# Kernel tuning notes

Measured on AMD Instinct MI355X. Metric: run time of the kernel, lower is better.

The kernel has to match this reference:

```python
import jax, jax.numpy as jnp
import numpy as np

NUM_EXPERTS = 8
TOP_K = 2
D = 2048   # hidden_dim
F = 4096   # ffn_dim


def setup_inputs() -> dict:
    key = jax.random.key(0)
    k0, k1, k2, k3, k4 = jax.random.split(key, 5)
    hidden_states = jax.random.normal(k0, (2, 2048, D), dtype=jnp.float32)
    gate_w = jax.random.normal(k1, (NUM_EXPERTS, D), dtype=jnp.float32) * 0.02
    w1 = jax.random.normal(k2, (NUM_EXPERTS, F, D), dtype=jnp.float32) * 0.02
    w2 = jax.random.normal(k3, (NUM_EXPERTS, D, F), dtype=jnp.float32) * 0.02
    w3 = jax.random.normal(k4, (NUM_EXPERTS, F, D), dtype=jnp.float32) * 0.02
    return {"hidden_states": hidden_states, "gate_w": gate_w, "w1": w1, "w2": w2, "w3": w3}


def reference(hidden_states, gate_w, w1, w2, w3):
    B, S, Dm = hidden_states.shape
    h = hidden_states.reshape(-1, Dm)                      # [T, D]
    router_logits = h @ gate_w.T                           # [T, E]
    rw = jax.nn.softmax(router_logits.astype(jnp.float32), axis=-1)
    rw, selected = jax.lax.top_k(rw, TOP_K)                # [T, K], [T, K]
    rw = rw / jnp.sum(rw, axis=-1, keepdims=True)
    rw = rw.astype(h.dtype)
    final = jnp.zeros_like(h)
    for e in range(NUM_EXPERTS):                            # small fixed loop over experts
        w = jnp.sum(rw * (selected == e), axis=1, keepdims=True)  # [T, 1]
        gated = jax.nn.silu(h @ w1[e].T) * (h @ w3[e].T)   # [T, F]
        final = final + (gated @ w2[e].T) * w              # [T, D]
    return final.reshape(B, S, Dm), router_logits
```

## Files before the change

kernel.cpp:

```cpp
#include <hip/hip_runtime.h>
#include <hip/hip_bf16.h>
#include <stdint.h>

#define NE 8
#define TKK 2
#define DD 2048
#define FF 4096
#define TT 4096
#define CONV13 2048
#define CONV2  1024

typedef __attribute__((ext_vector_type(8))) short bf16x8;
typedef __attribute__((ext_vector_type(4))) float f32x4;

__device__ inline unsigned short f2bf(float f) {
  union { float f; unsigned u; } x; x.f = f;
  unsigned r = x.u + 0x7fffu + ((x.u >> 16) & 1u);
  return (unsigned short)(r >> 16);
}

__device__ inline bf16x8 cvt8(float4 a, float4 b) {
  union { unsigned short h[8]; bf16x8 v; } x;
  x.h[0] = f2bf(a.x); x.h[1] = f2bf(a.y); x.h[2] = f2bf(a.z); x.h[3] = f2bf(a.w);
  x.h[4] = f2bf(b.x); x.h[5] = f2bf(b.y); x.h[6] = f2bf(b.z); x.h[7] = f2bf(b.w);
  return x.v;
}

__device__ __forceinline__ void conv8(const float* __restrict__ src,
                                      unsigned short* __restrict__ dst, long i) {
  float4 a = *(const float4*)(src + i);
  float4 b = *(const float4*)(src + i + 4);
  union { unsigned short h[8]; uint4 v; } o;
  o.h[0] = f2bf(a.x); o.h[1] = f2bf(a.y); o.h[2] = f2bf(a.z); o.h[3] = f2bf(a.w);
  o.h[4] = f2bf(b.x); o.h[5] = f2bf(b.y); o.h[6] = f2bf(b.z); o.h[7] = f2bf(b.w);
  *(uint4*)(dst + i) = o.v;
}

#define GLL16(g, l) __builtin_amdgcn_global_load_lds( \
    (__attribute__((address_space(1))) void*)(void*)(g), \
    (__attribute__((address_space(3))) void*)(l), 16, 0, 0)

__device__ __forceinline__ void router_one(
    int t, int lane, const float* __restrict__ h, const float* __restrict__ gw,
    float* __restrict__ logits, unsigned short* __restrict__ hb,
    int* __restrict__ counts, int* __restrict__ tok_idx,
    int* __restrict__ sel_e, int* __restrict__ sel_slot, float* __restrict__ sel_w) {
  const float4* hr = (const float4*)(h + (size_t)t * DD);
  float4 hv[8];
  float acc[NE];
#pragma unroll
  for (int e = 0; e < NE; e++) acc[e] = 0.f;
#pragma unroll
  for (int j = 0; j < 8; j++) hv[j] = hr[j * 64 + lane];
  ushort4* hbr = (ushort4*)(hb + (size_t)t * DD);
#pragma unroll
  for (int j = 0; j < 8; j++) {
    ushort4 o;
    o.x = f2bf(hv[j].x); o.y = f2bf(hv[j].y); o.z = f2bf(hv[j].z); o.w = f2bf(hv[j].w);
    hbr[j * 64 + lane] = o;
  }
#pragma unroll
  for (int e = 0; e < NE; e++) {
    const float4* g = (const float4*)(gw + (size_t)e * DD);
    float a = 0.f;
#pragma unroll
    for (int j = 0; j < 8; j++) {
      float4 gv = g[j * 64 + lane];
      a += hv[j].x * gv.x + hv[j].y * gv.y + hv[j].z * gv.z + hv[j].w * gv.w;
    }
    acc[e] = a;
  }
#pragma unroll
  for (int e = 0; e < NE; e++) {
    float v = acc[e];
#pragma unroll
    for (int o = 32; o > 0; o >>= 1) v += __shfl_xor(v, o, 64);
    acc[e] = v;
  }
  if (lane == 0) {
#pragma unroll
    for (int e = 0; e < NE; e++) logits[(size_t)t * NE + e] = acc[e];
    int e1 = 0; float m1 = acc[0];
#pragma unroll
    for (int e = 1; e < NE; e++) if (acc[e] > m1) { m1 = acc[e]; e1 = e; }
    int e2 = -1; float m2 = -3.4e38f;
#pragma unroll
    for (int e = 0; e < NE; e++) if (e != e1 && acc[e] > m2) { m2 = acc[e]; e2 = e; }
    float s = expf(m2 - m1);
    float wa = 1.f / (1.f + s);
    float wb = s * wa;
    int s1 = atomicAdd(&counts[e1], 1);
    tok_idx[e1 * TT + s1] = t;
    int s2 = atomicAdd(&counts[e2], 1);
    tok_idx[e2 * TT + s2] = t;
    sel_e[2 * t] = e1; sel_slot[2 * t] = s1; sel_w[2 * t] = wa;
    sel_e[2 * t + 1] = e2; sel_slot[2 * t + 1] = s2; sel_w[2 * t + 1] = wb;
  }
}

__global__ void router_kernel(const float* __restrict__ h, const float* __restrict__ gw,
                              float* __restrict__ logits, unsigned short* __restrict__ hb,
                              int* __restrict__ counts, int* __restrict__ tok_idx,
                              int* __restrict__ sel_e, int* __restrict__ sel_slot,
                              float* __restrict__ sel_w) {
  router_one(blockIdx.x, threadIdx.x, h, gw, logits, hb, counts, tok_idx, sel_e, sel_slot, sel_w);
}

__global__ __launch_bounds__(256) void prep_kernel(
    const float* __restrict__ h, const float* __restrict__ gw,
    float* __restrict__ logits, unsigned short* __restrict__ hb,
    int* __restrict__ counts, int* __restrict__ tok_idx,
    int* __restrict__ sel_e, int* __restrict__ sel_slot, float* __restrict__ sel_w,
    const float* __restrict__ w1, unsigned short* __restrict__ w1b,
    const float* __restrict__ w3, unsigned short* __restrict__ w3b) {
  if (blockIdx.x < CONV13) {
    long nw = (long)NE * FF * DD;
    long i = ((long)blockIdx.x * 256 + threadIdx.x) * 8;
    long stride = (long)CONV13 * 256 * 8;
    for (; i < 2 * nw; i += stride) {
      if (i < nw) conv8(w1, w1b, i);
      else        conv8(w3, w3b, i - nw);
    }
    return;
  }
  int b = blockIdx.x - CONV13;
  router_one(b * 4 + (threadIdx.x >> 6), threadIdx.x & 63,
             h, gw, logits, hb, counts, tok_idx, sel_e, sel_slot, sel_w);
}

__global__ void offsets_kernel(const int* __restrict__ counts, int* __restrict__ offsets) {
  if (threadIdx.x == 0) {
    int r = 0;
    for (int e = 0; e < NE; e++) { offsets[e] = r; r += counts[e]; }
  }
}

__global__ __launch_bounds__(256) void gemm1c_kernel(
    const unsigned short* __restrict__ w1b, const unsigned short* __restrict__ w3b,
    const unsigned short* __restrict__ hb, const int* __restrict__ tok_idx,
    const int* __restrict__ counts, const int* __restrict__ offsets,
    unsigned short* __restrict__ gated,
    const float* __restrict__ w2f, unsigned short* __restrict__ w2b) {
  __shared__ __align__(16) char lds[32768];
  char* Ab = lds;
  char* B1 = lds + 16384;
  char* B3 = lds + 24576;

  if (blockIdx.x < CONV2) {
    long nw = (long)NE * FF * DD;
    long i = ((long)blockIdx.x * 256 + threadIdx.x) * 8;
    long stride = (long)CONV2 * 256 * 8;
    for (; i < nw; i += stride) conv8(w2f, w2b, i);
    return;
  }

  int bid = blockIdx.x - CONV2;
  int x = bid & 7;
  int rest = bid >> 3;
  int m = rest & 31;
  int q = rest >> 5;
  int p = x + 8 * q;
  int n = p & 63;
  int e = p >> 6;
  int cnt = counts[e];
  int row0 = m * 128;
  if (row0 >= cnt) return;
  int offe = offsets[e];
  int tid = threadIdx.x;

  long asrc[4];
#pragma unroll
  for (int i = 0; i < 4; i++) {
    int r = i * 32 + (tid >> 3);
    int rr = row0 + r; if (rr >= cnt) rr = cnt - 1;
    int tok = tok_idx[e * TT + rr];
    asrc[i] = (long)tok * DD + (((tid & 7) ^ (r & 7)) * 8);
  }
  int fbase = n * 64;
  long ebase = (long)e * FF * DD;
  long bsrc[2];
#pragma unroll
  for (int i = 0; i < 2; i++) {
    int r = i * 32 + (tid >> 3);
    bsrc[i] = ebase + (long)(fbase + r) * DD + (((tid & 7) ^ (r & 7)) * 8);
  }

  f32x4 acc1[4][2], acc3[4][2];
#pragma unroll
  for (int i = 0; i < 4; i++)
#pragma unroll
    for (int j = 0; j < 2; j++) { acc1[i][j] = (f32x4){0,0,0,0}; acc3[i][j] = (f32x4){0,0,0,0}; }

  int wv = tid >> 6;
  int lane = tid & 63;
  int wr = (wv >> 1) * 64;
  int wc = (wv & 1) * 32;
  int lrow = lane & 15;
  int lk4 = lane >> 4;

  for (int k0 = 0; k0 < DD; k0 += 64) {
    if (k0) __syncthreads();
#pragma unroll
    for (int i = 0; i < 4; i++)
      GLL16(hb + asrc[i] + k0, Ab + i * 4096 + tid * 16);
#pragma unroll
    for (int i = 0; i < 2; i++) {
      GLL16(w1b + bsrc[i] + k0, B1 + i * 4096 + tid * 16);
      GLL16(w3b + bsrc[i] + k0, B3 + i * 4096 + tid * 16);
    }
    __syncthreads();
#pragma unroll
    for (int kk = 0; kk < 2; kk++) {
      int kseg = kk * 4 + lk4;
      bf16x8 af[4], b1f[2], b3f[2];
#pragma unroll
      for (int i = 0; i < 4; i++) {
        int row = wr + i * 16 + lrow;
        af[i] = *(const bf16x8*)(Ab + row * 128 + ((kseg ^ (row & 7)) * 16));
      }
#pragma unroll
      for (int j = 0; j < 2; j++) {
        int row = wc + j * 16 + lrow;
        int off = row * 128 + ((kseg ^ (row & 7)) * 16);
        b1f[j] = *(const bf16x8*)(B1 + off);
        b3f[j] = *(const bf16x8*)(B3 + off);
      }
#pragma unroll
      for (int i = 0; i < 4; i++)
#pragma unroll
        for (int j = 0; j < 2; j++) {
          acc1[i][j] = __builtin_amdgcn_mfma_f32_16x16x32_bf16(af[i], b1f[j], acc1[i][j], 0, 0, 0);
          acc3[i][j] = __builtin_amdgcn_mfma_f32_16x16x32_bf16(af[i], b3f[j], acc3[i][j], 0, 0, 0);
        }
    }
  }
  int crow0 = wr + (lane >> 4) * 4;
  int ccol0 = wc + (lane & 15);
#pragma unroll
  for (int i = 0; i < 4; i++)
#pragma unroll
    for (int j = 0; j < 2; j++)
#pragma unroll
      for (int r = 0; r < 4; r++) {
        int trow = crow0 + i * 16 + r;
        if (row0 + trow < cnt) {
          float g = acc1[i][j][r];
          float sg = g / (1.f + __expf(-g));
          float val = sg * acc3[i][j][r];
          gated[(size_t)(offe + row0 + trow) * FF + (fbase + ccol0 + j * 16)] = f2bf(val);
        }
      }
}

__global__ __launch_bounds__(256) void gemm1_kernel_fb(
    const float* __restrict__ w1f, const float* __restrict__ w3f,
    const unsigned short* __restrict__ hb, const int* __restrict__ tok_idx,
    const int* __restrict__ counts, const int* __restrict__ offsets,
    unsigned short* __restrict__ gated) {
  __shared__ __align__(16) char lds[49152];
  char* Ab = lds;
  char* B1 = lds + 16384;
  char* B3 = lds + 32768;

  int bid = blockIdx.x;
  int x = bid & 7;
  int rest = bid >> 3;
  int m = rest & 31;
  int q = rest >> 5;
  int p = x + 8 * q;
  int n = p & 63;
  int e = p >> 6;
  int cnt = counts[e];
  int row0 = m * 128;
  if (row0 >= cnt) return;
  int offe = offsets[e];
  int tid = threadIdx.x;

  long asrc[4];
#pragma unroll
  for (int i = 0; i < 4; i++) {
    int r = i * 32 + (tid >> 3);
    int rr = row0 + r; if (rr >= cnt) rr = cnt - 1;
    int tok = tok_idx[e * TT + rr];
    asrc[i] = (long)tok * DD + (((tid & 7) ^ (r & 7)) * 8);
  }
  int fbase = n * 64;
  long ebase = (long)e * FF * DD;
  long bsrc[4];
#pragma unroll
  for (int i = 0; i < 4; i++) {
    int r = i * 16 + (tid >> 4);
    bsrc[i] = ebase + (long)(fbase + r) * DD + (((tid & 15) ^ (r & 15)) * 4);
  }

  f32x4 acc1[4][2], acc3[4][2];
#pragma unroll
  for (int i = 0; i < 4; i++)
#pragma unroll
    for (int j = 0; j < 2; j++) { acc1[i][j] = (f32x4){0,0,0,0}; acc3[i][j] = (f32x4){0,0,0,0}; }

  int wv = tid >> 6;
  int lane = tid & 63;
  int wr = (wv >> 1) * 64;
  int wc = (wv & 1) * 32;
  int lrow = lane & 15;
  int lk4 = lane >> 4;

  for (int k0 = 0; k0 < DD; k0 += 64) {
    if (k0) __syncthreads();
#pragma unroll
    for (int i = 0; i < 4; i++)
      GLL16(hb + asrc[i] + k0, Ab + i * 4096 + tid * 16);
#pragma unroll
    for (int i = 0; i < 4; i++) {
      GLL16(w1f + bsrc[i] + k0, B1 + i * 4096 + tid * 16);
      GLL16(w3f + bsrc[i] + k0, B3 + i * 4096 + tid * 16);
    }
    __syncthreads();
#pragma unroll
    for (int kk = 0; kk < 2; kk++) {
      int kseg = kk * 4 + lk4;
      int fs = kk * 8 + lk4 * 2;
      bf16x8 af[4], b1f[2], b3f[2];
#pragma unroll
      for (int i = 0; i < 4; i++) {
        int row = wr + i * 16 + lrow;
        af[i] = *(const bf16x8*)(Ab + row * 128 + ((kseg ^ (row & 7)) * 16));
      }
#pragma unroll
      for (int j = 0; j < 2; j++) {
        int row = wc + j * 16 + lrow;
        int rx = row & 15;
        float4 a0 = *(const float4*)(B1 + row * 256 + ((fs ^ rx) * 16));
        float4 a1 = *(const float4*)(B1 + row * 256 + (((fs + 1) ^ rx) * 16));
        b1f[j] = cvt8(a0, a1);
        float4 c0 = *(const float4*)(B3 + row * 256 + ((fs ^ rx) * 16));
        float4 c1 = *(const float4*)(B3 + row * 256 + (((fs + 1) ^ rx) * 16));
        b3f[j] = cvt8(c0, c1);
      }
#pragma unroll
      for (int i = 0; i < 4; i++)
#pragma unroll
        for (int j = 0; j < 2; j++) {
          acc1[i][j] = __builtin_amdgcn_mfma_f32_16x16x32_bf16(af[i], b1f[j], acc1[i][j], 0, 0, 0);
          acc3[i][j] = __builtin_amdgcn_mfma_f32_16x16x32_bf16(af[i], b3f[j], acc3[i][j], 0, 0, 0);
        }
    }
  }
  int crow0 = wr + (lane >> 4) * 4;
  int ccol0 = wc + (lane & 15);
#pragma unroll
  for (int i = 0; i < 4; i++)
#pragma unroll
    for (int j = 0; j < 2; j++)
#pragma unroll
      for (int r = 0; r < 4; r++) {
        int trow = crow0 + i * 16 + r;
        if (row0 + trow < cnt) {
          float g = acc1[i][j][r];
          float sg = g / (1.f + __expf(-g));
          float val = sg * acc3[i][j][r];
          gated[(size_t)(offe + row0 + trow) * FF + (fbase + ccol0 + j * 16)] = f2bf(val);
        }
      }
}

template <bool WB16>
__global__ __launch_bounds__(256) void gemm2_kernel(
    const float* __restrict__ w2f, const unsigned short* __restrict__ w2b,
    const unsigned short* __restrict__ gated,
    const int* __restrict__ counts, const int* __restrict__ offsets,
    float* __restrict__ eout) {
  __shared__ __align__(16) char lds[WB16 ? 32768 : 49152];
  char* Ab = lds;
  char* Bb = lds + 16384;

  int bid = blockIdx.x;
  int x = bid & 7;
  int rest = bid >> 3;
  int m = rest & 31;
  int q = rest >> 5;
  int p = x + 8 * q;
  int n = p & 15;
  int e = p >> 4;
  int cnt = counts[e];
  int row0 = m * 128;
  if (row0 >= cnt) return;
  int offe = offsets[e];
  int tid = threadIdx.x;

  long asrc[4];
#pragma unroll
  for (int i = 0; i < 4; i++) {
    int r = i * 32 + (tid >> 3);
    int rr = row0 + r; if (rr >= cnt) rr = cnt - 1;
    asrc[i] = (long)(offe + rr) * FF + (((tid & 7) ^ (r & 7)) * 8);
  }
  int dbase = n * 128;
  long ebase = (long)e * DD * FF;
  long bsrc[8];
  if constexpr (WB16) {
#pragma unroll
    for (int i = 0; i < 4; i++) {
      int r = i * 32 + (tid >> 3);
      bsrc[i] = ebase + (long)(dbase + r) * FF + (((tid & 7) ^ (r & 7)) * 8);
    }
  } else {
#pragma unroll
    for (int i = 0; i < 8; i++) {
      int r = i * 16 + (tid >> 4);
      bsrc[i] = ebase + (long)(dbase + r) * FF + (((tid & 15) ^ (r & 15)) * 4);
    }
  }

  f32x4 acc[4][4];
#pragma unroll
  for (int i = 0; i < 4; i++)
#pragma unroll
    for (int j = 0; j < 4; j++) acc[i][j] = (f32x4){0,0,0,0};

  int wv = tid >> 6;
  int lane = tid & 63;
  int wr = (wv >> 1) * 64;
  int wc = (wv & 1) * 64;
  int lrow = lane & 15;
  int lk4 = lane >> 4;

  for (int k0 = 0; k0 < FF; k0 += 64) {
    if (k0) __syncthreads();
#pragma unroll
    for (int i = 0; i < 4; i++)
      GLL16(gated + asrc[i] + k0, Ab + i * 4096 + tid * 16);
    if constexpr (WB16) {
#pragma unroll
      for (int i = 0; i < 4; i++)
        GLL16(w2b + bsrc[i] + k0, Bb + i * 4096 + tid * 16);
    } else {
#pragma unroll
      for (int i = 0; i < 8; i++)
        GLL16(w2f + bsrc[i] + k0, Bb + i * 4096 + tid * 16);
    }
    __syncthreads();
#pragma unroll
    for (int kk = 0; kk < 2; kk++) {
      int kseg = kk * 4 + lk4;
      int fs = kk * 8 + lk4 * 2;
      bf16x8 af[4], bf[4];
#pragma unroll
      for (int i = 0; i < 4; i++) {
        int row = wr + i * 16 + lrow;
        af[i] = *(const bf16x8*)(Ab + row * 128 + ((kseg ^ (row & 7)) * 16));
      }
#pragma unroll
      for (int j = 0; j < 4; j++) {
        int row = wc + j * 16 + lrow;
        if constexpr (WB16) {
          bf[j] = *(const bf16x8*)(Bb + row * 128 + ((kseg ^ (row & 7)) * 16));
        } else {
          int rx = row & 15;
          float4 a0 = *(const float4*)(Bb + row * 256 + ((fs ^ rx) * 16));
          float4 a1 = *(const float4*)(Bb + row * 256 + (((fs + 1) ^ rx) * 16));
          bf[j] = cvt8(a0, a1);
        }
      }
#pragma unroll
      for (int i = 0; i < 4; i++)
#pragma unroll
        for (int j = 0; j < 4; j++)
          acc[i][j] = __builtin_amdgcn_mfma_f32_16x16x32_bf16(af[i], bf[j], acc[i][j], 0, 0, 0);
    }
  }
  int crow0 = wr + (lane >> 4) * 4;
  int ccol0 = wc + (lane & 15);
#pragma unroll
  for (int i = 0; i < 4; i++)
#pragma unroll
    for (int j = 0; j < 4; j++)
#pragma unroll
      for (int r = 0; r < 4; r++) {
        int trow = crow0 + i * 16 + r;
        if (row0 + trow < cnt)
          eout[(size_t)(offe + row0 + trow) * DD + (dbase + ccol0 + j * 16)] = acc[i][j][r];
      }
}

__global__ void gather_kernel(const float* __restrict__ eout, const int* __restrict__ offsets,
                              const int* __restrict__ sel_e, const int* __restrict__ sel_slot,
                              const float* __restrict__ sel_w, float* __restrict__ out) {
  int idx = blockIdx.x * 256 + threadIdx.x;
  int t = idx >> 9;
  int c = idx & 511;
  int ea = sel_e[2 * t], eb = sel_e[2 * t + 1];
  int sa = offsets[ea] + sel_slot[2 * t];
  int sb = offsets[eb] + sel_slot[2 * t + 1];
  float wa = sel_w[2 * t], wb = sel_w[2 * t + 1];
  float4 va = ((const float4*)(eout + (size_t)sa * DD))[c];
  float4 vb = ((const float4*)(eout + (size_t)sb * DD))[c];
  float4 o;
  o.x = wa * va.x + wb * vb.x;
  o.y = wa * va.y + wb * vb.y;
  o.z = wa * va.z + wb * vb.z;
  o.w = wa * va.w + wb * vb.w;
  ((float4*)(out + (size_t)t * DD))[c] = o;
}

extern "C" void kernel_launch(void* const* d_in, const int* in_sizes, int n_in,
                              void* d_out, int out_size, void* d_ws, size_t ws_size,
                              hipStream_t stream) {
  const float* h  = (const float*)d_in[0];
  const float* gw = (const float*)d_in[1];
  const float* w1 = (const float*)d_in[2];
  const float* w2 = (const float*)d_in[3];
  const float* w3 = (const float*)d_in[4];
  float* out = (float*)d_out;
  float* logits = out + (size_t)TT * DD;

  char* wp = (char*)d_ws;
  int* counts = (int*)wp; wp += 256;
  int* offsets = (int*)wp; wp += 256;
  int* tok_idx = (int*)wp; wp += (size_t)NE * TT * 4;
  int* sel_e = (int*)wp; wp += (size_t)TT * 2 * 4;
  int* sel_slot = (int*)wp; wp += (size_t)TT * 2 * 4;
  float* sel_w = (float*)wp; wp += (size_t)TT * 2 * 4;
  unsigned short* hb = (unsigned short*)wp; wp += (size_t)TT * DD * 2;
  unsigned short* gated = (unsigned short*)wp; wp += (size_t)TT * TKK * FF * 2;
  float* eout = (float*)wp; wp += (size_t)TT * TKK * DD * 4;
  if ((size_t)(wp - (char*)d_ws) > ws_size) return;

  long nw = (long)NE * FF * DD;
  unsigned short* w1b = (unsigned short*)wp; wp += (size_t)nw * 2;
  unsigned short* w3b = (unsigned short*)wp; wp += (size_t)nw * 2;
  unsigned short* w2b = (unsigned short*)wp; wp += (size_t)nw * 2;
  bool wb16 = ((size_t)(wp - (char*)d_ws) <= ws_size);

  hipMemsetAsync(counts, 0, 32, stream);
  if (wb16) {
    prep_kernel<<<CONV13 + TT / 4, 256, 0, stream>>>(
        h, gw, logits, hb, counts, tok_idx, sel_e, sel_slot, sel_w, w1, w1b, w3, w3b);
    offsets_kernel<<<1, 64, 0, stream>>>(counts, offsets);
    gemm1c_kernel<<<CONV2 + 8 * 32 * 64, 256, 0, stream>>>(
        w1b, w3b, hb, tok_idx, counts, offsets, gated, w2, w2b);
    gemm2_kernel<true><<<8 * 32 * 16, 256, 0, stream>>>(w2, w2b, gated, counts, offsets, eout);
  } else {
    router_kernel<<<TT, 64, 0, stream>>>(h, gw, logits, hb, counts, tok_idx, sel_e, sel_slot, sel_w);
    offsets_kernel<<<1, 64, 0, stream>>>(counts, offsets);
    gemm1_kernel_fb<<<8 * 32 * 64, 256, 0, stream>>>(w1, w3, hb, tok_idx, counts, offsets, gated);
    gemm2_kernel<false><<<8 * 32 * 16, 256, 0, stream>>>(w2, nullptr, gated, counts, offsets, eout);
  }
  gather_kernel<<<(TT * DD / 4) / 256, 256, 0, stream>>>(eout, offsets, sel_e, sel_slot, sel_w, out);
}
```

Before: 850.0 us.

## Replace expert GEMMs with 256x128 double-buffered 8-phase pipelined MFMA kernels

Rewrites both expert GEMMs as 512-thread kernels with 256x128 tiles. Each kernel double-buffers its LDS stages and interleaves the global->LDS loads for the next K-step with MFMA phases, using raw barriers, waitcnt and setprio. The w2 fp32->bf16 conversion moves from the GEMM1 launch into the prep kernel alongside w1/w3. The intent is to hide load latency and raise reuse per tile. The cost is large LDS use (128KB for GEMM1), which likely allows only one block per CU, plus fewer blocks for small expert counts.

```diff
diff --git a/kernel.cpp b/kernel.cpp
--- a/kernel.cpp
+++ b/kernel.cpp
@@ -7,8 +7,7 @@
 #define DD 2048
 #define FF 4096
 #define TT 4096
-#define CONV13 2048
-#define CONV2  1024
+#define CONVP 3072
 
 typedef __attribute__((ext_vector_type(8))) short bf16x8;
 typedef __attribute__((ext_vector_type(4))) float f32x4;
@@ -39,6 +38,11 @@
 #define GLL16(g, l) __builtin_amdgcn_global_load_lds( \
     (__attribute__((address_space(1))) void*)(void*)(g), \
     (__attribute__((address_space(3))) void*)(l), 16, 0, 0)
+
+#define LDV(p) (*(const bf16x8*)(p))
+#define MF(d, a, b) d = __builtin_amdgcn_mfma_f32_16x16x32_bf16(a, b, d, 0, 0, 0)
+#define BARPH() do { asm volatile("" ::: "memory"); __builtin_amdgcn_s_barrier(); \
+                     __builtin_amdgcn_sched_barrier(0); } while (0)
 
 __device__ __forceinline__ void router_one(
     int t, int lane, const float* __restrict__ h, const float* __restrict__ gw,
@@ -112,18 +116,20 @@
     int* __restrict__ counts, int* __restrict__ tok_idx,
     int* __restrict__ sel_e, int* __restrict__ sel_slot, float* __restrict__ sel_w,
     const float* __restrict__ w1, unsigned short* __restrict__ w1b,
-    const float* __restrict__ w3, unsigned short* __restrict__ w3b) {
-  if (blockIdx.x < CONV13) {
+    const float* __restrict__ w3, unsigned short* __restrict__ w3b,
+    const float* __restrict__ w2, unsigned short* __restrict__ w2b) {
+  if (blockIdx.x < CONVP) {
     long nw = (long)NE * FF * DD;
     long i = ((long)blockIdx.x * 256 + threadIdx.x) * 8;
-    long stride = (long)CONV13 * 256 * 8;
-    for (; i < 2 * nw; i += stride) {
-      if (i < nw) conv8(w1, w1b, i);
-      else        conv8(w3, w3b, i - nw);
+    long stride = (long)CONVP * 256 * 8;
+    for (; i < 3 * nw; i += stride) {
+      if (i < nw)          conv8(w1, w1b, i);
+      else if (i < 2 * nw) conv8(w3, w3b, i - nw);
+      else                 conv8(w2, w2b, i - 2 * nw);
     }
     return;
   }
-  int b = blockIdx.x - CONV13;
+  int b = blockIdx.x - CONVP;
   router_one(b * 4 + (threadIdx.x >> 6), threadIdx.x & 63,
              h, gw, logits, hb, counts, tok_idx, sel_e, sel_slot, sel_w);
 }
@@ -135,120 +141,273 @@
   }
 }
 
-__global__ __launch_bounds__(256) void gemm1c_kernel(
+
+__global__ __launch_bounds__(512, 2) void gemm1_8p(
     const unsigned short* __restrict__ w1b, const unsigned short* __restrict__ w3b,
     const unsigned short* __restrict__ hb, const int* __restrict__ tok_idx,
     const int* __restrict__ counts, const int* __restrict__ offsets,
-    unsigned short* __restrict__ gated,
-    const float* __restrict__ w2f, unsigned short* __restrict__ w2b) {
-  __shared__ __align__(16) char lds[32768];
-  char* Ab = lds;
-  char* B1 = lds + 16384;
-  char* B3 = lds + 24576;
-
-  if (blockIdx.x < CONV2) {
-    long nw = (long)NE * FF * DD;
-    long i = ((long)blockIdx.x * 256 + threadIdx.x) * 8;
-    long stride = (long)CONV2 * 256 * 8;
-    for (; i < nw; i += stride) conv8(w2f, w2b, i);
-    return;
-  }
-
-  int bid = blockIdx.x - CONV2;
-  int x = bid & 7;
-  int rest = bid >> 3;
-  int m = rest & 31;
-  int q = rest >> 5;
+    unsigned short* __restrict__ gated) {
+  __shared__ __align__(16) char lds[131072];
+
+  int bid = blockIdx.x;
+  int x = bid & 7, rest = bid >> 3;
+  int m = rest & 15, q = rest >> 4;
   int p = x + 8 * q;
-  int n = p & 63;
-  int e = p >> 6;
+  int n = p & 31, e = p >> 5;
   int cnt = counts[e];
-  int row0 = m * 128;
+  int row0 = m * 256;
   if (row0 >= cnt) return;
   int offe = offsets[e];
   int tid = threadIdx.x;
-
+  int lane = tid & 63;
+  int wv = tid >> 6;
+  int wm = wv >> 2, wn = wv & 3;
+
+  int swz = ((tid & 7) ^ ((tid >> 3) & 7)) * 8;
   long asrc[4];
 #pragma unroll
   for (int i = 0; i < 4; i++) {
-    int r = i * 32 + (tid >> 3);
+    int r = i * 64 + (tid >> 3);
     int rr = row0 + r; if (rr >= cnt) rr = cnt - 1;
     int tok = tok_idx[e * TT + rr];
-    asrc[i] = (long)tok * DD + (((tid & 7) ^ (r & 7)) * 8);
-  }
-  int fbase = n * 64;
-  long ebase = (long)e * FF * DD;
-  long bsrc[2];
+    asrc[i] = (long)tok * DD + swz;
+  }
+  int fbase = n * 128;
+  long ebw = (long)e * FF * DD;
+  long bs[2];
 #pragma unroll
   for (int i = 0; i < 2; i++) {
-    int r = i * 32 + (tid >> 3);
-    bsrc[i] = ebase + (long)(fbase + r) * DD + (((tid & 7) ^ (r & 7)) * 8);
-  }
-
-  f32x4 acc1[4][2], acc3[4][2];
-#pragma unroll
-  for (int i = 0; i < 4; i++)
+    int r = i * 64 + (tid >> 3);
+    bs[i] = ebw + (long)(fbase + r) * DD + swz;
+  }
+
+#define G1A(c, i, ko)  GLL16(hb  + asrc[i] + (ko), lds +           (c) * 32768 + (i) * 8192 + tid * 16)
+#define G1B1(c, i, ko) GLL16(w1b + bs[i]   + (ko), lds + 65536 +  (c) * 16384 + (i) * 8192 + tid * 16)
+#define G1B3(c, i, ko) GLL16(w3b + bs[i]   + (ko), lds + 98304 +  (c) * 16384 + (i) * 8192 + tid * 16)
+
+  int arow[8], brow[2];
+#pragma unroll
+  for (int i = 0; i < 8; i++) arow[i] = (wm * 128 + i * 16 + (lane & 15)) * 128;
+#pragma unroll
+  for (int j = 0; j < 2; j++) brow[j] = (wn * 32 + j * 16 + (lane & 15)) * 128;
+  int kx0 = (((lane >> 4)) ^ (lane & 7)) * 16;
+  int kx1 = ((4 + (lane >> 4)) ^ (lane & 7)) * 16;
+
+  f32x4 acc1[8][2], acc3[8][2];
+#pragma unroll
+  for (int i = 0; i < 8; i++)
 #pragma unroll
     for (int j = 0; j < 2; j++) { acc1[i][j] = (f32x4){0,0,0,0}; acc3[i][j] = (f32x4){0,0,0,0}; }
 
-  int wv = tid >> 6;
-  int lane = tid & 63;
-  int wr = (wv >> 1) * 64;
-  int wc = (wv & 1) * 32;
-  int lrow = lane & 15;
-  int lk4 = lane >> 4;
-
-  for (int k0 = 0; k0 < DD; k0 += 64) {
-    if (k0) __syncthreads();
-#pragma unroll
-    for (int i = 0; i < 4; i++)
-      GLL16(hb + asrc[i] + k0, Ab + i * 4096 + tid * 16);
-#pragma unroll
-    for (int i = 0; i < 2; i++) {
-      GLL16(w1b + bsrc[i] + k0, B1 + i * 4096 + tid * 16);
-      GLL16(w3b + bsrc[i] + k0, B3 + i * 4096 + tid * 16);
-    }
-    __syncthreads();
-#pragma unroll
-    for (int kk = 0; kk < 2; kk++) {
-      int kseg = kk * 4 + lk4;
-      bf16x8 af[4], b1f[2], b3f[2];
-#pragma unroll
-      for (int i = 0; i < 4; i++) {
-        int row = wr + i * 16 + lrow;
-        af[i] = *(const bf16x8*)(Ab + row * 128 + ((kseg ^ (row & 7)) * 16));
-      }
-#pragma unroll
-      for (int j = 0; j < 2; j++) {
-        int row = wc + j * 16 + lrow;
-        int off = row * 128 + ((kseg ^ (row & 7)) * 16);
-        b1f[j] = *(const bf16x8*)(B1 + off);
-        b3f[j] = *(const bf16x8*)(B3 + off);
-      }
-#pragma unroll
-      for (int i = 0; i < 4; i++)
-#pragma unroll
-        for (int j = 0; j < 2; j++) {
-          acc1[i][j] = __builtin_amdgcn_mfma_f32_16x16x32_bf16(af[i], b1f[j], acc1[i][j], 0, 0, 0);
-          acc3[i][j] = __builtin_amdgcn_mfma_f32_16x16x32_bf16(af[i], b3f[j], acc3[i][j], 0, 0, 0);
-        }
-    }
-  }
-  int crow0 = wr + (lane >> 4) * 4;
-  int ccol0 = wc + (lane & 15);
-#pragma unroll
-  for (int i = 0; i < 4; i++)
+  G1A(0, 0, 0); G1A(0, 2, 0);
+  G1B1(0, 0, 0); G1B1(0, 1, 0);
+  G1B3(0, 0, 0); G1B3(0, 1, 0);
+  G1A(0, 1, 0); G1A(0, 3, 0);
+
+  int cur = 0;
+  bf16x8 b10, b11, b30, b31;
+  for (int kt = 0; kt < DD / 64; kt++) {
+    int ko = (kt + 1) * 64;
+    bool st = (kt < DD / 64 - 1);
+    int nc = cur ^ 1;
+    const char* Ac  = lds + cur * 32768;
+    const char* B1c = lds + 65536 + cur * 16384;
+    const char* B3c = lds + 98304 + cur * 16384;
+
+    asm volatile("s_waitcnt vmcnt(2)" ::: "memory");
+    BARPH();
+    if (st) { G1A(nc, 0, ko); G1A(nc, 2, ko); }
+    b10 = LDV(B1c + brow[0] + kx0); b11 = LDV(B1c + brow[1] + kx0);
+    b30 = LDV(B3c + brow[0] + kx0); b31 = LDV(B3c + brow[1] + kx0);
+    __builtin_amdgcn_s_setprio(1);
+#pragma unroll
+    for (int i = 0; i < 4; i++) {
+      bf16x8 av = LDV(Ac + arow[i] + kx0);
+      MF(acc1[i][0], av, b10); MF(acc1[i][1], av, b11);
+      MF(acc3[i][0], av, b30); MF(acc3[i][1], av, b31);
+    }
+    __builtin_amdgcn_s_setprio(0);
+
+    if (st) asm volatile("s_waitcnt vmcnt(2)" ::: "memory");
+    else    asm volatile("s_waitcnt vmcnt(0)" ::: "memory");
+    BARPH();
+    if (st) { G1B1(nc, 0, ko); G1B1(nc, 1, ko); }
+    __builtin_amdgcn_s_setprio(1);
+#pragma unroll
+    for (int i = 4; i < 8; i++) {
+      bf16x8 av = LDV(Ac + arow[i] + kx0);
+      MF(acc1[i][0], av, b10); MF(acc1[i][1], av, b11);
+      MF(acc3[i][0], av, b30); MF(acc3[i][1], av, b31);
+    }
+    __builtin_amdgcn_s_setprio(0);
+
+    BARPH();
+    if (st) { G1B3(nc, 0, ko); G1B3(nc, 1, ko); }
+    b10 = LDV(B1c + brow[0] + kx1); b11 = LDV(B1c + brow[1] + kx1);
+    b30 = LDV(B3c + brow[0] + kx1); b31 = LDV(B3c + brow[1] + kx1);
+    __builtin_amdgcn_s_setprio(1);
+#pragma unroll
+    for (int i = 0; i < 4; i++) {
+      bf16x8 av = LDV(Ac + arow[i] + kx1);
+      MF(acc1[i][0], av, b10); MF(acc1[i][1], av, b11);
+      MF(acc3[i][0], av, b30); MF(acc3[i][1], av, b31);
+    }
+    __builtin_amdgcn_s_setprio(0);
+
+    BARPH();
+    if (st) { G1A(nc, 1, ko); G1A(nc, 3, ko); }
+    __builtin_amdgcn_s_setprio(1);
+#pragma unroll
+    for (int i = 4; i < 8; i++) {
+      bf16x8 av = LDV(Ac + arow[i] + kx1);
+      MF(acc1[i][0], av, b10); MF(acc1[i][1], av, b11);
+      MF(acc3[i][0], av, b30); MF(acc3[i][1], av, b31);
+    }
+    __builtin_amdgcn_s_setprio(0);
+    cur = nc;
+  }
+
+  int r0 = wm * 128 + ((lane >> 4) << 2);
+  int c0 = fbase + wn * 32 + (lane & 15);
+#pragma unroll
+  for (int i = 0; i < 8; i++)
 #pragma unroll
     for (int j = 0; j < 2; j++)
 #pragma unroll
       for (int r = 0; r < 4; r++) {
-        int trow = crow0 + i * 16 + r;
-        if (row0 + trow < cnt) {
+        int tr = r0 + i * 16 + r;
+        if (row0 + tr < cnt) {
           float g = acc1[i][j][r];
           float sg = g / (1.f + __expf(-g));
-          float val = sg * acc3[i][j][r];
-          gated[(size_t)(offe + row0 + trow) * FF + (fbase + ccol0 + j * 16)] = f2bf(val);
+          gated[(size_t)(offe + row0 + tr) * FF + (c0 + j * 16)] = f2bf(sg * acc3[i][j][r]);
         }
+      }
+}
+
+__global__ __launch_bounds__(512, 2) void gemm2_8p(
+    const unsigned short* __restrict__ w2b, const unsigned short* __restrict__ gated,
+    const int* __restrict__ counts, const int* __restrict__ offsets,
+    float* __restrict__ eout) {
+  __shared__ __align__(16) char lds[98304];
+
+  int bid = blockIdx.x;
+  int x = bid & 7, rest = bid >> 3;
+  int m = rest & 15, q = rest >> 4;
+  int p = x + 8 * q;
+  int n = p & 15, e = p >> 4;
+  int cnt = counts[e];
+  int row0 = m * 256;
+  if (row0 >= cnt) return;
+  int offe = offsets[e];
+  int tid = threadIdx.x;
+  int lane = tid & 63;
+  int wv = tid >> 6;
+  int wm = wv >> 2, wn = wv & 3;
+
+  int swz = ((tid & 7) ^ ((tid >> 3) & 7)) * 8;
+  long asrc[4];
+#pragma unroll
+  for (int i = 0; i < 4; i++) {
+    int r = i * 64 + (tid >> 3);
+    int rr = row0 + r; if (rr >= cnt) rr = cnt - 1;
+    asrc[i] = (long)(offe + rr) * FF + swz;
+  }
+  int dbase = n * 128;
+  long ebw = (long)e * DD * FF;
+  long bs[2];
+#pragma unroll
+  for (int i = 0; i < 2; i++) {
+    int r = i * 64 + (tid >> 3);
+    bs[i] = ebw + (long)(dbase + r) * FF + swz;
+  }
+
+#define G2A(c, i, ko) GLL16(gated + asrc[i] + (ko), lds +          (c) * 32768 + (i) * 8192 + tid * 16)
+#define G2B(c, i, ko) GLL16(w2b   + bs[i]   + (ko), lds + 65536 + (c) * 16384 + (i) * 8192 + tid * 16)
+
+  int arow[8], brow[2];
+#pragma unroll
+  for (int i = 0; i < 8; i++) arow[i] = (wm * 128 + i * 16 + (lane & 15)) * 128;
+#pragma unroll
+  for (int j = 0; j < 2; j++) brow[j] = (wn * 32 + j * 16 + (lane & 15)) * 128;
+  int kx0 = (((lane >> 4)) ^ (lane & 7)) * 16;
+  int kx1 = ((4 + (lane >> 4)) ^ (lane & 7)) * 16;
+
+  f32x4 acc[8][2];
+#pragma unroll
+  for (int i = 0; i < 8; i++)
+#pragma unroll
+    for (int j = 0; j < 2; j++) acc[i][j] = (f32x4){0,0,0,0};
+
+  G2A(0, 0, 0); G2A(0, 2, 0);
+  G2B(0, 0, 0); G2B(0, 1, 0);
+  G2A(0, 1, 0); G2A(0, 3, 0);
+
+  int cur = 0;
+  bf16x8 b0, b1;
+  for (int kt = 0; kt < FF / 64; kt++) {
+    int ko = (kt + 1) * 64;
+    bool st = (kt < FF / 64 - 1);
+    int nc = cur ^ 1;
+    const char* Ac = lds + cur * 32768;
+    const char* Bc = lds + 65536 + cur * 16384;
+
+    asm volatile("s_waitcnt vmcnt(2)" ::: "memory");
+    BARPH();
+    if (st) { G2A(nc, 0, ko); G2A(nc, 2, ko); }
+    b0 = LDV(Bc + brow[0] + kx0); b1 = LDV(Bc + brow[1] + kx0);
+    __builtin_amdgcn_s_setprio(1);
+#pragma unroll
+    for (int i = 0; i < 4; i++) {
+      bf16x8 av = LDV(Ac + arow[i] + kx0);
+      MF(acc[i][0], av, b0); MF(acc[i][1], av, b1);
+    }
+    __builtin_amdgcn_s_setprio(0);
+
+    if (st) asm volatile("s_waitcnt vmcnt(2)" ::: "memory");
+    else    asm volatile("s_waitcnt vmcnt(0)" ::: "memory");
+    BARPH();
+    if (st) { G2B(nc, 0, ko); G2B(nc, 1, ko); }
+    __builtin_amdgcn_s_setprio(1);
+#pragma unroll
+    for (int i = 4; i < 8; i++) {
+      bf16x8 av = LDV(Ac + arow[i] + kx0);
+      MF(acc[i][0], av, b0); MF(acc[i][1], av, b1);
+    }
+    __builtin_amdgcn_s_setprio(0);
+
+    BARPH();
+    if (st) { G2A(nc, 1, ko); G2A(nc, 3, ko); }
+    b0 = LDV(Bc + brow[0] + kx1); b1 = LDV(Bc + brow[1] + kx1);
+    __builtin_amdgcn_s_setprio(1);
+#pragma unroll
+    for (int i = 0; i < 4; i++) {
+      bf16x8 av = LDV(Ac + arow[i] + kx1);
+      MF(acc[i][0], av, b0); MF(acc[i][1], av, b1);
+    }
+    __builtin_amdgcn_s_setprio(0);
+
+    BARPH();
+    __builtin_amdgcn_s_setprio(1);
+#pragma unroll
+    for (int i = 4; i < 8; i++) {
+      bf16x8 av = LDV(Ac + arow[i] + kx1);
+      MF(acc[i][0], av, b0); MF(acc[i][1], av, b1);
+    }
+    __builtin_amdgcn_s_setprio(0);
+    cur = nc;
+  }
+
+  int r0 = wm * 128 + ((lane >> 4) << 2);
+  int c0 = dbase + wn * 32 + (lane & 15);
+#pragma unroll
+  for (int i = 0; i < 8; i++)
+#pragma unroll
+    for (int j = 0; j < 2; j++)
+#pragma unroll
+      for (int r = 0; r < 4; r++) {
+        int tr = r0 + i * 16 + r;
+        if (row0 + tr < cnt)
+          eout[(size_t)(offe + row0 + tr) * DD + (c0 + j * 16)] = acc[i][j][r];
       }
 }
 
@@ -365,13 +524,11 @@
       }
 }
 
-template <bool WB16>
-__global__ __launch_bounds__(256) void gemm2_kernel(
-    const float* __restrict__ w2f, const unsigned short* __restrict__ w2b,
-    const unsigned short* __restrict__ gated,
+__global__ __launch_bounds__(256) void gemm2_kernel_fb(
+    const float* __restrict__ w2f, const unsigned short* __restrict__ gated,
     const int* __restrict__ counts, const int* __restrict__ offsets,
     float* __restrict__ eout) {
-  __shared__ __align__(16) char lds[WB16 ? 32768 : 49152];
+  __shared__ __align__(16) char lds[49152];
   char* Ab = lds;
   char* Bb = lds + 16384;
 
@@ -399,18 +556,10 @@
   int dbase = n * 128;
   long ebase = (long)e * DD * FF;
   long bsrc[8];
-  if constexpr (WB16) {
-#pragma unroll
-    for (int i = 0; i < 4; i++) {
-      int r = i * 32 + (tid >> 3);
-      bsrc[i] = ebase + (long)(dbase + r) * FF + (((tid & 7) ^ (r & 7)) * 8);
-    }
-  } else {
-#pragma unroll
-    for (int i = 0; i < 8; i++) {
-      int r = i * 16 + (tid >> 4);
-      bsrc[i] = ebase + (long)(dbase + r) * FF + (((tid & 15) ^ (r & 15)) * 4);
-    }
+#pragma unroll
+  for (int i = 0; i < 8; i++) {
+    int r = i * 16 + (tid >> 4);
+    bsrc[i] = ebase + (long)(dbase + r) * FF + (((tid & 15) ^ (r & 15)) * 4);
   }
 
   f32x4 acc[4][4];
@@ -431,15 +580,9 @@
 #pragma unroll
     for (int i = 0; i < 4; i++)
       GLL16(gated + asrc[i] + k0, Ab + i * 4096 + tid * 16);
-    if constexpr (WB16) {
-#pragma unroll
-      for (int i = 0; i < 4; i++)
-        GLL16(w2b + bsrc[i] + k0, Bb + i * 4096 + tid * 16);
-    } else {
-#pragma unroll
-      for (int i = 0; i < 8; i++)
-        GLL16(w2f + bsrc[i] + k0, Bb + i * 4096 + tid * 16);
-    }
+#pragma unroll
+    for (int i = 0; i < 8; i++)
+      GLL16(w2f + bsrc[i] + k0, Bb + i * 4096 + tid * 16);
     __syncthreads();
 #pragma unroll
     for (int kk = 0; kk < 2; kk++) {
@@ -454,14 +597,10 @@
 #pragma unroll
       for (int j = 0; j < 4; j++) {
         int row = wc + j * 16 + lrow;
-        if constexpr (WB16) {
-          bf[j] = *(const bf16x8*)(Bb + row * 128 + ((kseg ^ (row & 7)) * 16));
-        } else {
-          int rx = row & 15;
-          float4 a0 = *(const float4*)(Bb + row * 256 + ((fs ^ rx) * 16));
-          float4 a1 = *(const float4*)(Bb + row * 256 + (((fs + 1) ^ rx) * 16));
-          bf[j] = cvt8(a0, a1);
-        }
+        int rx = row & 15;
+        float4 a0 = *(const float4*)(Bb + row * 256 + ((fs ^ rx) * 16));
+        float4 a1 = *(const float4*)(Bb + row * 256 + (((fs + 1) ^ rx) * 16));
+        bf[j] = cvt8(a0, a1);
       }
 #pragma unroll
       for (int i = 0; i < 4; i++)
@@ -535,17 +674,17 @@
 
   hipMemsetAsync(counts, 0, 32, stream);
   if (wb16) {
-    prep_kernel<<<CONV13 + TT / 4, 256, 0, stream>>>(
-        h, gw, logits, hb, counts, tok_idx, sel_e, sel_slot, sel_w, w1, w1b, w3, w3b);
+    prep_kernel<<<CONVP + TT / 4, 256, 0, stream>>>(
+        h, gw, logits, hb, counts, tok_idx, sel_e, sel_slot, sel_w,
+        w1, w1b, w3, w3b, w2, w2b);
     offsets_kernel<<<1, 64, 0, stream>>>(counts, offsets);
-    gemm1c_kernel<<<CONV2 + 8 * 32 * 64, 256, 0, stream>>>(
-        w1b, w3b, hb, tok_idx, counts, offsets, gated, w2, w2b);
-    gemm2_kernel<true><<<8 * 32 * 16, 256, 0, stream>>>(w2, w2b, gated, counts, offsets, eout);
+    gemm1_8p<<<8 * 16 * 32, 512, 0, stream>>>(w1b, w3b, hb, tok_idx, counts, offsets, gated);
+    gemm2_8p<<<8 * 16 * 16, 512, 0, stream>>>(w2b, gated, counts, offsets, eout);
   } else {
     router_kernel<<<TT, 64, 0, stream>>>(h, gw, logits, hb, counts, tok_idx, sel_e, sel_slot, sel_w);
     offsets_kernel<<<1, 64, 0, stream>>>(counts, offsets);
     gemm1_kernel_fb<<<8 * 32 * 64, 256, 0, stream>>>(w1, w3, hb, tok_idx, counts, offsets, gated);
-    gemm2_kernel<false><<<8 * 32 * 16, 256, 0, stream>>>(w2, nullptr, gated, counts, offsets, eout);
+    gemm2_kernel_fb<<<8 * 32 * 16, 256, 0, stream>>>(w2, gated, counts, offsets, eout);
   }
   gather_kernel<<<(TT * DD / 4) / 256, 256, 0, stream>>>(eout, offsets, sel_e, sel_slot, sel_w, out);
 }
```

Measured after the change: 903.5 us. 1.06x slower.
